# Kernel optimization log

Hardware: AMD Instinct MI355X
Metric: run time of the kernel (lower is better)

## Reference

```python
import jax, jax.numpy as jnp
import numpy as np

B, S, H = 2, 4096, 2048
NUM_HEADS = 32
HEAD_DIM = H // NUM_HEADS  # 64
SCALE = 1.0 / (HEAD_DIM ** 0.5)
D2 = H // 2  # complex rotation dim per the module (full hidden, not per-head)


def setup_inputs() -> dict:
    key = jax.random.key(0)
    ks = jax.random.split(key, 6)
    hidden_states = jax.random.normal(ks[0], (B, S, H), dtype=jnp.float32)
    init = 0.02  # keep logits in a sane range like trained weights
    wq = jax.random.normal(ks[1], (H, H), dtype=jnp.float32) * init
    wk = jax.random.normal(ks[2], (H, H), dtype=jnp.float32) * init
    wv = jax.random.normal(ks[3], (H, H), dtype=jnp.float32) * init
    wo = jax.random.normal(ks[4], (H, H), dtype=jnp.float32) * init
    # standard RoPE frequency table over the D2 complex lanes
    inv_freq = 1.0 / (10000.0 ** (jnp.arange(D2, dtype=jnp.float32) / D2))
    angles = jnp.arange(S, dtype=jnp.float32)[:, None] * inv_freq[None, :]  # [S, D2]
    freqs_cos = jnp.cos(angles)
    freqs_sin = jnp.sin(angles)
    position_ids = jnp.arange(S, dtype=jnp.int64)
    return {
        "hidden_states": hidden_states,
        "wq": wq, "wk": wk, "wv": wv, "wo": wo,
        "freqs_cos": freqs_cos, "freqs_sin": freqs_sin,
        "position_ids": position_ids,
    }


def _rope(x, cos, sin):
    # x: [B, S, H]; complex pair split at H//2 (module-level, not per-head)
    xr, xi = x[..., :D2], x[..., D2:]
    out_r = xr * cos - xi * sin
    out_i = xr * sin + xi * cos
    # torch.view_as_real(...).flatten(2) interleaves (re, im) pairs
    return jnp.stack([out_r, out_i], axis=-1).reshape(x.shape)


def reference(hidden_states, wq, wk, wv, wo, freqs_cos, freqs_sin, position_ids):
    q = jnp.einsum('bsh,oh->bso', hidden_states, wq)
    k = jnp.einsum('bsh,oh->bso', hidden_states, wk)
    v = jnp.einsum('bsh,oh->bso', hidden_states, wv)
    cos = freqs_cos[position_ids]  # [S, D2]
    sin = freqs_sin[position_ids]
    q_rot = _rope(q, cos, sin)
    k_rot = _rope(k, cos, sin)
    scores = jnp.einsum('bqd,bkd->bqk', q_rot, k_rot) * SCALE  # [B, S, S]
    probs = jax.nn.softmax(scores, axis=-1)
    ctx = jnp.einsum('bqk,bkd->bqd', probs, v)
    output = jnp.einsum('bsh,oh->bso', ctx, wo)
    return output, k_rot, v
```

## Files before the change

### kernel.cpp

```cpp
#include <hip/hip_runtime.h>
#include <cstdint>
#include <cstddef>

#define B_    2
#define S_    4096
#define H_    2048
#define D2_   1024
#define SCALE_ 0.125f

typedef __attribute__((ext_vector_type(8))) _Float16 half8;
typedef __attribute__((ext_vector_type(4))) float f32x4;

__device__ __forceinline__ ushort f2h(float f) {
    _Float16 h = (_Float16)f;
    return *(ushort*)&h;
}
__device__ __forceinline__ float h2f(ushort u) {
    return (float)(*(_Float16*)&u);
}

__device__ __forceinline__ void gld_lds16(const ushort* g, ushort* l) {
    __builtin_amdgcn_global_load_lds((const __attribute__((address_space(1))) void*)g,
                                     (__attribute__((address_space(3))) void*)l,
                                     16, 0, 0);
}

__global__ __launch_bounds__(256) void cast_f16_kernel(const float* __restrict__ src,
                                                       ushort* __restrict__ dst, int n4) {
    int i = blockIdx.x * 256 + threadIdx.x;
    if (i < n4) {
        float4 v = ((const float4*)src)[i];
        ushort4 o;
        o.x = f2h(v.x); o.y = f2h(v.y); o.z = f2h(v.z); o.w = f2h(v.w);
        ((ushort4*)dst)[i] = o;
    }
}

__global__ __launch_bounds__(256) void cast4_f16_kernel(const float* __restrict__ w0,
                                                        const float* __restrict__ w1,
                                                        const float* __restrict__ w2,
                                                        const float* __restrict__ w3,
                                                        ushort* __restrict__ o0,
                                                        ushort* __restrict__ o1,
                                                        ushort* __restrict__ o2,
                                                        ushort* __restrict__ o3,
                                                        int n4) {
    int i = blockIdx.x * 256 + threadIdx.x;
    if (i >= n4) return;
    const float* s; ushort* d;
    switch (blockIdx.y) {
        case 0: s = w0; d = o0; break;
        case 1: s = w1; d = o1; break;
        case 2: s = w2; d = o2; break;
        default: s = w3; d = o3; break;
    }
    float4 v = ((const float4*)s)[i];
    ushort4 o;
    o.x = f2h(v.x); o.y = f2h(v.y); o.z = f2h(v.z); o.w = f2h(v.w);
    ((ushort4*)d)[i] = o;
}

#define WAIT_VM(N) asm volatile("s_waitcnt vmcnt(" #N ")" ::: "memory")
#define BAR        asm volatile("s_barrier" ::: "memory")

template <int QM>
__device__ __forceinline__ void ld_a(const ushort* pA, int aRow0, int kx0, int kx1,
                                     half8 (&af)[4][2]) {
#pragma unroll
    for (int mi = 0; mi < 4; mi++) {
        af[mi][0] = *(const half8*)(pA + aRow0 + QM * 4096 + mi * 1024 + kx0);
        af[mi][1] = *(const half8*)(pA + aRow0 + QM * 4096 + mi * 1024 + kx1);
    }
}
template <int QN>
__device__ __forceinline__ void ld_b(const ushort* pB, int bRow0, int kx0, int kx1,
                                     half8 (&bf)[2][2]) {
#pragma unroll
    for (int ni = 0; ni < 2; ni++) {
        bf[ni][0] = *(const half8*)(pB + bRow0 + QN * 2048 + ni * 1024 + kx0);
        bf[ni][1] = *(const half8*)(pB + bRow0 + QN * 2048 + ni * 1024 + kx1);
    }
}
template <int QM, int QN>
__device__ __forceinline__ void mma(const half8 (&af)[4][2], const half8 (&bf)[2][2],
                                    f32x4 (&acc)[8][4]) {
    __builtin_amdgcn_s_setprio(1);
#pragma unroll
    for (int mi = 0; mi < 4; mi++)
#pragma unroll
        for (int ni = 0; ni < 2; ni++) {
            f32x4 c = acc[QM * 4 + mi][QN * 2 + ni];
            c = __builtin_amdgcn_mfma_f32_16x16x32_f16(af[mi][0], bf[ni][0], c, 0, 0, 0);
            c = __builtin_amdgcn_mfma_f32_16x16x32_f16(af[mi][1], bf[ni][1], c, 0, 0, 0);
            acc[QM * 4 + mi][QN * 2 + ni] = c;
        }
    __builtin_amdgcn_s_setprio(0);
}

template <bool HALF_OUT>
__global__ __launch_bounds__(512, 1) void gemm256(const ushort* __restrict__ A,
                                                  const ushort* __restrict__ B,
                                                  void* __restrict__ Cv,
                                                  int M, int N, int K, float alpha,
                                                  size_t sA, size_t sB, size_t sC) {
    __shared__ __align__(16) ushort As[2][256][64];
    __shared__ __align__(16) ushort Bs[2][256][64];

    A += (size_t)blockIdx.z * sA;
    B += (size_t)blockIdx.z * sB;

    const int nwg  = gridDim.x * gridDim.y;
    const int orig = blockIdx.y * gridDim.x + blockIdx.x;
    const int wg   = (orig & 7) * (nwg >> 3) + (orig >> 3);
    const int bm   = (wg / gridDim.x) * 256;
    const int bn   = (wg % gridDim.x) * 256;

    const int tid  = threadIdx.x;
    const int lane = tid & 63;
    const int wave = tid >> 6;
    const int wr   = wave >> 2;
    const int wc   = wave & 3;
    const int col  = lane & 15;
    const int quad = lane >> 4;

    const int srow = tid >> 3;
    const int scol = ((tid & 7) ^ (srow & 7)) * 8;
    const ushort* gA = A + (size_t)(bm + srow) * K + scol;
    const ushort* gB = B + (size_t)(bn + srow) * K + scol;
    const size_t rs64  = (size_t)64 * K;
    const size_t rs128 = (size_t)128 * K;
    ushort* lA = &As[0][0][0] + tid * 8;
    ushort* lB = &Bs[0][0][0] + tid * 8;

    auto stA = [&](int t, int h) {
        const ushort* s = gA + (size_t)t * 64 + (h ? rs128 : (size_t)0);
        ushort* d = lA + ((t & 1) << 14) + (h << 13);
        gld_lds16(s, d);
        gld_lds16(s + rs64, d + 4096);
    };
    auto stB = [&](int t, int h) {
        const ushort* s = gB + (size_t)t * 64 + (h ? rs128 : (size_t)0);
        ushort* d = lB + ((t & 1) << 14) + (h << 13);
        gld_lds16(s, d);
        gld_lds16(s + rs64, d + 4096);
    };

    const int kx0   = ((quad ^ (col & 7)) * 8);
    const int kx1   = (((4 + quad) ^ (col & 7)) * 8);
    const int aRow0 = (wr * 128 + col) * 64;
    const int bRow0 = (wc * 64 + col) * 64;
    const ushort* pAs = &As[0][0][0];
    const ushort* pBs = &Bs[0][0][0];

    f32x4 acc[8][4];
#pragma unroll
    for (int i = 0; i < 8; i++)
#pragma unroll
        for (int j = 0; j < 4; j++) { f32x4 z = {0.f, 0.f, 0.f, 0.f}; acc[i][j] = z; }

    half8 af0[4][2], af1[4][2], bf0[2][2], bf1[2][2];

    const int T = K >> 6;

    stA(0, 0); stA(0, 1); stB(0, 0); stB(0, 1);

    for (int t = 0; t < T; ++t) {
        const int bo = (t & 1) << 14;

        WAIT_VM(4);
        BAR;
        ld_a<0>(pAs + bo, aRow0, kx0, kx1, af0);
        if (t + 1 < T) { stA(t + 1, 0); stA(t + 1, 1); }
        if (t > 0) mma<1, 0>(af1, bf0, acc);

        if (t + 1 < T) { WAIT_VM(4); }
        else           { WAIT_VM(0); }
        BAR;
        if (t > 0) mma<1, 1>(af1, bf1, acc);
        ld_b<0>(pBs + bo, bRow0, kx0, kx1, bf0);
        ld_b<1>(pBs + bo, bRow0, kx0, kx1, bf1);
        if (t + 1 < T) { stB(t + 1, 0); stB(t + 1, 1); }
        ld_a<1>(pAs + bo, aRow0, kx0, kx1, af1);
        mma<0, 0>(af0, bf0, acc);
        mma<0, 1>(af0, bf1, acc);
    }
    mma<1, 0>(af1, bf0, acc);
    mma<1, 1>(af1, bf1, acc);

    ushort* Ch = (ushort*)Cv + (size_t)blockIdx.z * sC;
    float*  Cf = (float*)Cv + (size_t)blockIdx.z * sC;
#pragma unroll
    for (int qm = 0; qm < 2; qm++)
#pragma unroll
        for (int mi = 0; mi < 4; mi++)
#pragma unroll
            for (int qn = 0; qn < 2; qn++)
#pragma unroll
                for (int ni = 0; ni < 2; ni++)
#pragma unroll
                    for (int r = 0; r < 4; r++) {
                        int grow = bm + wr * 128 + qm * 64 + mi * 16 + quad * 4 + r;
                        int gcol = bn + wc * 64 + qn * 32 + ni * 16 + col;
                        float val = alpha * acc[qm * 4 + mi][qn * 2 + ni][r];
                        if (HALF_OUT)
                            Ch[(size_t)grow * N + gcol] = f2h(val);
                        else
                            Cf[(size_t)grow * N + gcol] = val;
                    }
}

__global__ __launch_bounds__(256) void rope_kernel(const ushort* __restrict__ qh,
                                                   const ushort* __restrict__ kh,
                                                   const float* __restrict__ cosT,
                                                   const float* __restrict__ sinT,
                                                   const int* __restrict__ pos,
                                                   ushort* __restrict__ qr,
                                                   ushort* __restrict__ kr,
                                                   float* __restrict__ krf32) {
    int idx = blockIdx.x * 256 + threadIdx.x;
    int row = idx >> 8;
    int jj  = (idx & 255) * 4;
    int p = pos[row & (S_ - 1)];
    const ushort* q = qh + (size_t)row * H_ + jj;
    const ushort* k = kh + (size_t)row * H_ + jj;
    const float* cr = cosT + (size_t)p * D2_ + jj;
    const float* sr = sinT + (size_t)p * D2_ + jj;
    float4 c = *(const float4*)cr;
    float4 sn = *(const float4*)sr;
    ushort4 qr4 = *(const ushort4*)q;
    ushort4 qi4 = *(const ushort4*)(q + D2_);
    ushort4 kr4 = *(const ushort4*)k;
    ushort4 ki4 = *(const ushort4*)(k + D2_);

    float qrv[4] = {h2f(qr4.x), h2f(qr4.y), h2f(qr4.z), h2f(qr4.w)};
    float qiv[4] = {h2f(qi4.x), h2f(qi4.y), h2f(qi4.z), h2f(qi4.w)};
    float krv[4] = {h2f(kr4.x), h2f(kr4.y), h2f(kr4.z), h2f(kr4.w)};
    float kiv[4] = {h2f(ki4.x), h2f(ki4.y), h2f(ki4.z), h2f(ki4.w)};
    float cv[4] = {c.x, c.y, c.z, c.w};
    float sv[4] = {sn.x, sn.y, sn.z, sn.w};

    ushort qo[8], ko[8];
    float kf[8];
#pragma unroll
    for (int t = 0; t < 4; t++) {
        float o0 = qrv[t] * cv[t] - qiv[t] * sv[t];
        float o1 = qrv[t] * sv[t] + qiv[t] * cv[t];
        qo[2 * t] = f2h(o0); qo[2 * t + 1] = f2h(o1);
        float p0 = krv[t] * cv[t] - kiv[t] * sv[t];
        float p1 = krv[t] * sv[t] + kiv[t] * cv[t];
        ko[2 * t] = f2h(p0); ko[2 * t + 1] = f2h(p1);
        kf[2 * t] = p0; kf[2 * t + 1] = p1;
    }
    ushort* qro = qr + (size_t)row * H_ + 2 * jj;
    ushort* kro = kr + (size_t)row * H_ + 2 * jj;
    float* krf  = krf32 + (size_t)row * H_ + 2 * jj;
    *(ushort4*)(qro)     = *(ushort4*)(qo);
    *(ushort4*)(qro + 4) = *(ushort4*)(qo + 4);
    *(ushort4*)(kro)     = *(ushort4*)(ko);
    *(ushort4*)(kro + 4) = *(ushort4*)(ko + 4);
    *(float4*)(krf)      = *(float4*)(kf);
    *(float4*)(krf + 4)  = *(float4*)(kf + 4);
}

__global__ __launch_bounds__(256) void transpose_cast_kernel(const float* __restrict__ v,
                                                             ushort* __restrict__ vt) {
    __shared__ float tile[32][33];
    int b  = blockIdx.z;
    int s0 = blockIdx.y * 32, h0 = blockIdx.x * 32;
    const float* vb = v + (size_t)b * S_ * H_;
    ushort* vtb = vt + (size_t)b * H_ * S_;
    int tx = threadIdx.x & 31, ty = threadIdx.x >> 5;
#pragma unroll
    for (int i = 0; i < 32; i += 8)
        tile[ty + i][tx] = vb[(size_t)(s0 + ty + i) * H_ + h0 + tx];
    __syncthreads();
#pragma unroll
    for (int i = 0; i < 32; i += 8)
        vtb[(size_t)(h0 + ty + i) * S_ + s0 + tx] = f2h(tile[tx][ty + i]);
}

__global__ __launch_bounds__(256) void softmax_kernel(const float* __restrict__ sc,
                                                      ushort* __restrict__ pr) {
    __shared__ float red[8];
    size_t row = blockIdx.x;
    const float4* r = (const float4*)(sc + row * (size_t)S_);
    int tid = threadIdx.x;
    float4 v[4];
    float m = -1e30f;
#pragma unroll
    for (int i = 0; i < 4; i++) {
        v[i] = r[tid + i * 256];
        m = fmaxf(m, fmaxf(fmaxf(v[i].x, v[i].y), fmaxf(v[i].z, v[i].w)));
    }
#pragma unroll
    for (int off = 32; off >= 1; off >>= 1) m = fmaxf(m, __shfl_xor(m, off));
    if ((tid & 63) == 0) red[tid >> 6] = m;
    __syncthreads();
    m = fmaxf(fmaxf(red[0], red[1]), fmaxf(red[2], red[3]));
    float s = 0.f;
#pragma unroll
    for (int i = 0; i < 4; i++) {
        v[i].x = __expf(v[i].x - m); v[i].y = __expf(v[i].y - m);
        v[i].z = __expf(v[i].z - m); v[i].w = __expf(v[i].w - m);
        s += v[i].x + v[i].y + v[i].z + v[i].w;
    }
#pragma unroll
    for (int off = 32; off >= 1; off >>= 1) s += __shfl_xor(s, off);
    if ((tid & 63) == 0) red[4 + (tid >> 6)] = s;
    __syncthreads();
    float inv = 1.0f / (red[4] + red[5] + red[6] + red[7]);
    ushort4* o = (ushort4*)(pr + row * (size_t)S_);
#pragma unroll
    for (int i = 0; i < 4; i++) {
        ushort4 u;
        u.x = f2h(v[i].x * inv); u.y = f2h(v[i].y * inv);
        u.z = f2h(v[i].z * inv); u.w = f2h(v[i].w * inv);
        o[tid + i * 256] = u;
    }
}

extern "C" void kernel_launch(void* const* d_in, const int* in_sizes, int n_in,
                              void* d_out, int out_size, void* d_ws, size_t ws_size,
                              hipStream_t stream) {
    const float* hs   = (const float*)d_in[0];
    const float* wq   = (const float*)d_in[1];
    const float* wk   = (const float*)d_in[2];
    const float* wv   = (const float*)d_in[3];
    const float* wo   = (const float*)d_in[4];
    const float* fcos = (const float*)d_in[5];
    const float* fsin = (const float*)d_in[6];
    const int*   pos  = (const int*)d_in[7];

    const size_t BSH = (size_t)B_ * S_ * H_;
    const size_t HH  = (size_t)H_ * H_;

    float* out      = (float*)d_out;
    float* krot_out = out + BSH;
    float* v_out    = krot_out + BSH;

    char* ws = (char*)d_ws;
    const size_t MB = 1ull << 20;
    ushort* Xb  = (ushort*)(ws + 0);
    ushort* Wqb = (ushort*)(ws + 32 * MB);
    ushort* Wkb = (ushort*)(ws + 40 * MB);
    ushort* Wvb = (ushort*)(ws + 48 * MB);
    ushort* Wob = (ushort*)(ws + 56 * MB);
    ushort* qh  = (ushort*)(ws + 64 * MB);
    ushort* kh  = (ushort*)(ws + 96 * MB);
    ushort* qrb = (ushort*)(ws + 128 * MB);
    ushort* krb = (ushort*)(ws + 160 * MB);
    ushort* vtb = (ushort*)(ws + 192 * MB);
    float*  sc  = (float*)(ws + 224 * MB);
    ushort* prb = (ushort*)(ws + 64 * MB);
    ushort* cb  = (ushort*)(ws + 128 * MB);

    cast_f16_kernel<<<(int)(BSH / 4 / 256), 256, 0, stream>>>(hs, Xb, (int)(BSH / 4));
    cast4_f16_kernel<<<dim3((int)(HH / 4 / 256), 4), 256, 0, stream>>>(
        wq, wk, wv, wo, Wqb, Wkb, Wvb, Wob, (int)(HH / 4));

    dim3 gProj(H_ / 256, (B_ * S_) / 256, 1);
    gemm256<true ><<<gProj, 512, 0, stream>>>(Xb, Wqb, qh,    B_ * S_, H_, H_, 1.0f, 0, 0, 0);
    gemm256<true ><<<gProj, 512, 0, stream>>>(Xb, Wkb, kh,    B_ * S_, H_, H_, 1.0f, 0, 0, 0);
    gemm256<false><<<gProj, 512, 0, stream>>>(Xb, Wvb, v_out, B_ * S_, H_, H_, 1.0f, 0, 0, 0);

    rope_kernel<<<(B_ * S_ * (D2_ / 4)) / 256, 256, 0, stream>>>(
        qh, kh, fcos, fsin, pos, qrb, krb, krot_out);

    transpose_cast_kernel<<<dim3(H_ / 32, S_ / 32, B_), 256, 0, stream>>>(v_out, vtb);

    dim3 gSc(S_ / 256, S_ / 256, B_);
    gemm256<false><<<gSc, 512, 0, stream>>>(qrb, krb, sc, S_, S_, H_, SCALE_,
                                            (size_t)S_ * H_, (size_t)S_ * H_,
                                            (size_t)S_ * S_);

    softmax_kernel<<<B_ * S_, 256, 0, stream>>>(sc, prb);

    dim3 gPV(H_ / 256, S_ / 256, B_);
    gemm256<true><<<gPV, 512, 0, stream>>>(prb, vtb, cb, S_, H_, S_, 1.0f,
                                           (size_t)S_ * S_, (size_t)H_ * S_,
                                           (size_t)S_ * H_);

    gemm256<false><<<gProj, 512, 0, stream>>>(cb, Wob, out, B_ * S_, H_, H_, 1.0f, 0, 0, 0);
}
```

Before: 855.9 us.

## Switch GEMM to 32x32x16 MFMA, unroll tile steps, store scores in fp16

The GEMM inner loop now uses 32x32x16 MFMA instructions with 16-wide accumulators and new LDS fragment addressing, in place of 16x16x32 tiles. The main loop is unrolled by two so the buffer index becomes a compile-time constant. Separately, the score matrix is written as fp16 instead of fp32 and softmax reads fp16, halving score memory traffic. The fp16 scores add precision and overflow risk, and the loop unroll assumes an even K/64 tile count.

```diff
diff --git a/kernel.cpp b/kernel.cpp
--- a/kernel.cpp
+++ b/kernel.cpp
@@ -10,6 +10,7 @@
 
 typedef __attribute__((ext_vector_type(8))) _Float16 half8;
 typedef __attribute__((ext_vector_type(4))) float f32x4;
+typedef __attribute__((ext_vector_type(16))) float f32x16;
 
 __device__ __forceinline__ ushort f2h(float f) {
     _Float16 h = (_Float16)f;
@@ -63,39 +64,50 @@
 #define WAIT_VM(N) asm volatile("s_waitcnt vmcnt(" #N ")" ::: "memory")
 #define BAR        asm volatile("s_barrier" ::: "memory")
 
-template <int QM>
-__device__ __forceinline__ void ld_a(const ushort* pA, int aRow0, int kx0, int kx1,
-                                     half8 (&af)[4][2]) {
-#pragma unroll
-    for (int mi = 0; mi < 4; mi++) {
-        af[mi][0] = *(const half8*)(pA + aRow0 + QM * 4096 + mi * 1024 + kx0);
-        af[mi][1] = *(const half8*)(pA + aRow0 + QM * 4096 + mi * 1024 + kx1);
-    }
-}
-template <int QN>
-__device__ __forceinline__ void ld_b(const ushort* pB, int bRow0, int kx0, int kx1,
-                                     half8 (&bf)[2][2]) {
-#pragma unroll
-    for (int ni = 0; ni < 2; ni++) {
-        bf[ni][0] = *(const half8*)(pB + bRow0 + QN * 2048 + ni * 1024 + kx0);
-        bf[ni][1] = *(const half8*)(pB + bRow0 + QN * 2048 + ni * 1024 + kx1);
-    }
+template <int BUF, int QM>
+__device__ __forceinline__ void ldA(const ushort* const (&aP)[4], half8 (&af)[2][4]) {
+#pragma unroll
+    for (int m2 = 0; m2 < 2; m2++)
+#pragma unroll
+        for (int ks = 0; ks < 4; ks++)
+            af[m2][ks] = *(const half8*)(aP[ks] + BUF * 16384 + (QM * 2 + m2) * 2048);
+}
+template <int BUF, int QN>
+__device__ __forceinline__ void ldB(const ushort* const (&bP)[4], half8 (&bf)[4]) {
+#pragma unroll
+    for (int ks = 0; ks < 4; ks++)
+        bf[ks] = *(const half8*)(bP[ks] + BUF * 16384 + QN * 2048);
 }
 template <int QM, int QN>
-__device__ __forceinline__ void mma(const half8 (&af)[4][2], const half8 (&bf)[2][2],
-                                    f32x4 (&acc)[8][4]) {
+__device__ __forceinline__ void mma32(const half8 (&af)[2][4], const half8 (&bf)[4],
+                                      f32x16 (&acc)[4][2]) {
     __builtin_amdgcn_s_setprio(1);
 #pragma unroll
-    for (int mi = 0; mi < 4; mi++)
-#pragma unroll
-        for (int ni = 0; ni < 2; ni++) {
-            f32x4 c = acc[QM * 4 + mi][QN * 2 + ni];
-            c = __builtin_amdgcn_mfma_f32_16x16x32_f16(af[mi][0], bf[ni][0], c, 0, 0, 0);
-            c = __builtin_amdgcn_mfma_f32_16x16x32_f16(af[mi][1], bf[ni][1], c, 0, 0, 0);
-            acc[QM * 4 + mi][QN * 2 + ni] = c;
-        }
+    for (int ks = 0; ks < 4; ks++)
+#pragma unroll
+        for (int m2 = 0; m2 < 2; m2++)
+            acc[QM * 2 + m2][QN] = __builtin_amdgcn_mfma_f32_32x32x16_f16(
+                af[m2][ks], bf[ks], acc[QM * 2 + m2][QN], 0, 0, 0);
     __builtin_amdgcn_s_setprio(0);
 }
+
+#define TILE_STEP(T_, BUF_, STG_, LASTY_, DOPREV_)                      \
+    {                                                                   \
+        WAIT_VM(4);                                                     \
+        BAR;                                                            \
+        ldA<BUF_, 0>(aP, af0);                                          \
+        if (STG_) { stA((T_) + 1, 0); stA((T_) + 1, 1); }               \
+        if (DOPREV_) mma32<1, 0>(af1, bf0, acc);                        \
+        if (LASTY_) { WAIT_VM(0); } else { WAIT_VM(4); }                \
+        BAR;                                                            \
+        if (DOPREV_) mma32<1, 1>(af1, bf1, acc);                        \
+        ldB<BUF_, 0>(bP, bf0);                                          \
+        ldB<BUF_, 1>(bP, bf1);                                          \
+        if (STG_) { stB((T_) + 1, 0); stB((T_) + 1, 1); }               \
+        ldA<BUF_, 1>(aP, af1);                                          \
+        mma32<0, 0>(af0, bf0, acc);                                     \
+        mma32<0, 1>(af0, bf1, acc);                                     \
+    }
 
 template <bool HALF_OUT>
 __global__ __launch_bounds__(512, 1) void gemm256(const ushort* __restrict__ A,
@@ -120,8 +132,9 @@
     const int wave = tid >> 6;
     const int wr   = wave >> 2;
     const int wc   = wave & 3;
-    const int col  = lane & 15;
-    const int quad = lane >> 4;
+    const int r32  = lane & 31;
+    const int kh   = lane >> 5;
+    const int xk   = r32 & 7;
 
     const int srow = tid >> 3;
     const int scol = ((tid & 7) ^ (srow & 7)) * 8;
@@ -145,68 +158,57 @@
         gld_lds16(s + rs64, d + 4096);
     };
 
-    const int kx0   = ((quad ^ (col & 7)) * 8);
-    const int kx1   = (((4 + quad) ^ (col & 7)) * 8);
-    const int aRow0 = (wr * 128 + col) * 64;
-    const int bRow0 = (wc * 64 + col) * 64;
-    const ushort* pAs = &As[0][0][0];
-    const ushort* pBs = &Bs[0][0][0];
-
-    f32x4 acc[8][4];
-#pragma unroll
-    for (int i = 0; i < 8; i++)
-#pragma unroll
-        for (int j = 0; j < 4; j++) { f32x4 z = {0.f, 0.f, 0.f, 0.f}; acc[i][j] = z; }
-
-    half8 af0[4][2], af1[4][2], bf0[2][2], bf1[2][2];
-
-    const int T = K >> 6;
+    int kq[4];
+#pragma unroll
+    for (int ks = 0; ks < 4; ks++) kq[ks] = ((ks * 2 + kh) ^ xk) * 8;
+    const ushort* aP[4];
+    const ushort* bP[4];
+#pragma unroll
+    for (int ks = 0; ks < 4; ks++) {
+        aP[ks] = &As[0][0][0] + (wr * 128 + r32) * 64 + kq[ks];
+        bP[ks] = &Bs[0][0][0] + (wc * 64 + r32) * 64 + kq[ks];
+    }
+
+    f32x16 acc[4][2];
+#pragma unroll
+    for (int i = 0; i < 4; i++)
+#pragma unroll
+        for (int j = 0; j < 2; j++)
+#pragma unroll
+            for (int r = 0; r < 16; r++) acc[i][j][r] = 0.f;
+
+    half8 af0[2][4], af1[2][4], bf0[4], bf1[4];
+
+    const int T  = K >> 6;
+    const int TP = T >> 1;
 
     stA(0, 0); stA(0, 1); stB(0, 0); stB(0, 1);
 
-    for (int t = 0; t < T; ++t) {
-        const int bo = (t & 1) << 14;
-
-        WAIT_VM(4);
-        BAR;
-        ld_a<0>(pAs + bo, aRow0, kx0, kx1, af0);
-        if (t + 1 < T) { stA(t + 1, 0); stA(t + 1, 1); }
-        if (t > 0) mma<1, 0>(af1, bf0, acc);
-
-        if (t + 1 < T) { WAIT_VM(4); }
-        else           { WAIT_VM(0); }
-        BAR;
-        if (t > 0) mma<1, 1>(af1, bf1, acc);
-        ld_b<0>(pBs + bo, bRow0, kx0, kx1, bf0);
-        ld_b<1>(pBs + bo, bRow0, kx0, kx1, bf1);
-        if (t + 1 < T) { stB(t + 1, 0); stB(t + 1, 1); }
-        ld_a<1>(pAs + bo, aRow0, kx0, kx1, af1);
-        mma<0, 0>(af0, bf0, acc);
-        mma<0, 1>(af0, bf1, acc);
-    }
-    mma<1, 0>(af1, bf0, acc);
-    mma<1, 1>(af1, bf1, acc);
+    for (int p = 0; p < TP; ++p) {
+        const int t0 = 2 * p;
+        TILE_STEP(t0,     0, true,        false,       t0 > 0);
+        TILE_STEP(t0 + 1, 1, p + 1 < TP,  p + 1 == TP, true);
+    }
+    mma32<1, 0>(af1, bf0, acc);
+    mma32<1, 1>(af1, bf1, acc);
 
     ushort* Ch = (ushort*)Cv + (size_t)blockIdx.z * sC;
     float*  Cf = (float*)Cv + (size_t)blockIdx.z * sC;
 #pragma unroll
-    for (int qm = 0; qm < 2; qm++)
-#pragma unroll
-        for (int mi = 0; mi < 4; mi++)
-#pragma unroll
-            for (int qn = 0; qn < 2; qn++)
-#pragma unroll
-                for (int ni = 0; ni < 2; ni++)
-#pragma unroll
-                    for (int r = 0; r < 4; r++) {
-                        int grow = bm + wr * 128 + qm * 64 + mi * 16 + quad * 4 + r;
-                        int gcol = bn + wc * 64 + qn * 32 + ni * 16 + col;
-                        float val = alpha * acc[qm * 4 + mi][qn * 2 + ni][r];
-                        if (HALF_OUT)
-                            Ch[(size_t)grow * N + gcol] = f2h(val);
-                        else
-                            Cf[(size_t)grow * N + gcol] = val;
-                    }
+    for (int mt = 0; mt < 4; mt++)
+#pragma unroll
+        for (int nt = 0; nt < 2; nt++) {
+            const int gcol = bn + wc * 64 + nt * 32 + r32;
+#pragma unroll
+            for (int reg = 0; reg < 16; reg++) {
+                int grow = bm + wr * 128 + mt * 32 + (reg & 3) + 8 * (reg >> 2) + 4 * kh;
+                float val = alpha * acc[mt][nt][reg];
+                if (HALF_OUT)
+                    Ch[(size_t)grow * N + gcol] = f2h(val);
+                else
+                    Cf[(size_t)grow * N + gcol] = val;
+            }
+        }
 }
 
 __global__ __launch_bounds__(256) void rope_kernel(const ushort* __restrict__ qh,
@@ -279,19 +281,23 @@
         vtb[(size_t)(h0 + ty + i) * S_ + s0 + tx] = f2h(tile[tx][ty + i]);
 }
 
-__global__ __launch_bounds__(256) void softmax_kernel(const float* __restrict__ sc,
+__global__ __launch_bounds__(256) void softmax_kernel(const ushort* __restrict__ sc,
                                                       ushort* __restrict__ pr) {
     __shared__ float red[8];
     size_t row = blockIdx.x;
-    const float4* r = (const float4*)(sc + row * (size_t)S_);
+    const uint4* r = (const uint4*)(sc + row * (size_t)S_);
     int tid = threadIdx.x;
-    float4 v[4];
+    uint4 v0 = r[tid], v1 = r[tid + 256];
+    uint w[8] = {v0.x, v0.y, v0.z, v0.w, v1.x, v1.y, v1.z, v1.w};
+    float f[16];
+#pragma unroll
+    for (int i = 0; i < 8; i++) {
+        f[2 * i]     = h2f((ushort)(w[i] & 0xffffu));
+        f[2 * i + 1] = h2f((ushort)(w[i] >> 16));
+    }
     float m = -1e30f;
 #pragma unroll
-    for (int i = 0; i < 4; i++) {
-        v[i] = r[tid + i * 256];
-        m = fmaxf(m, fmaxf(fmaxf(v[i].x, v[i].y), fmaxf(v[i].z, v[i].w)));
-    }
+    for (int i = 0; i < 16; i++) m = fmaxf(m, f[i]);
 #pragma unroll
     for (int off = 32; off >= 1; off >>= 1) m = fmaxf(m, __shfl_xor(m, off));
     if ((tid & 63) == 0) red[tid >> 6] = m;
@@ -299,24 +305,22 @@
     m = fmaxf(fmaxf(red[0], red[1]), fmaxf(red[2], red[3]));
     float s = 0.f;
 #pragma unroll
-    for (int i = 0; i < 4; i++) {
-        v[i].x = __expf(v[i].x - m); v[i].y = __expf(v[i].y - m);
-        v[i].z = __expf(v[i].z - m); v[i].w = __expf(v[i].w - m);
-        s += v[i].x + v[i].y + v[i].z + v[i].w;
-    }
+    for (int i = 0; i < 16; i++) { f[i] = __expf(f[i] - m); s += f[i]; }
 #pragma unroll
     for (int off = 32; off >= 1; off >>= 1) s += __shfl_xor(s, off);
     if ((tid & 63) == 0) red[4 + (tid >> 6)] = s;
     __syncthreads();
     float inv = 1.0f / (red[4] + red[5] + red[6] + red[7]);
-    ushort4* o = (ushort4*)(pr + row * (size_t)S_);
-#pragma unroll
-    for (int i = 0; i < 4; i++) {
-        ushort4 u;
-        u.x = f2h(v[i].x * inv); u.y = f2h(v[i].y * inv);
-        u.z = f2h(v[i].z * inv); u.w = f2h(v[i].w * inv);
-        o[tid + i * 256] = u;
-    }
+    uint o[8];
+#pragma unroll
+    for (int i = 0; i < 8; i++)
+        o[i] = (uint)f2h(f[2 * i] * inv) | ((uint)f2h(f[2 * i + 1] * inv) << 16);
+    uint4* op = (uint4*)(pr + row * (size_t)S_);
+    uint4 u0, u1;
+    u0.x = o[0]; u0.y = o[1]; u0.z = o[2]; u0.w = o[3];
+    u1.x = o[4]; u1.y = o[5]; u1.z = o[6]; u1.w = o[7];
+    op[tid] = u0;
+    op[tid + 256] = u1;
 }
 
 extern "C" void kernel_launch(void* const* d_in, const int* in_sizes, int n_in,
@@ -350,7 +354,7 @@
     ushort* qrb = (ushort*)(ws + 128 * MB);
     ushort* krb = (ushort*)(ws + 160 * MB);
     ushort* vtb = (ushort*)(ws + 192 * MB);
-    float*  sc  = (float*)(ws + 224 * MB);
+    ushort* sc  = (ushort*)(ws + 224 * MB);
     ushort* prb = (ushort*)(ws + 64 * MB);
     ushort* cb  = (ushort*)(ws + 128 * MB);
 
@@ -369,9 +373,9 @@
     transpose_cast_kernel<<<dim3(H_ / 32, S_ / 32, B_), 256, 0, stream>>>(v_out, vtb);
 
     dim3 gSc(S_ / 256, S_ / 256, B_);
-    gemm256<false><<<gSc, 512, 0, stream>>>(qrb, krb, sc, S_, S_, H_, SCALE_,
-                                            (size_t)S_ * H_, (size_t)S_ * H_,
-                                            (size_t)S_ * S_);
+    gemm256<true><<<gSc, 512, 0, stream>>>(qrb, krb, sc, S_, S_, H_, SCALE_,
+                                           (size_t)S_ * H_, (size_t)S_ * H_,
+                                           (size_t)S_ * S_);
 
     softmax_kernel<<<B_ * S_, 256, 0, stream>>>(sc, prb);
 
```

After: 1.113 ms. 1.3x slower.
